# Performance work log

Measured on AMD Instinct MI355X. Metric: run time of the kernel, lower is better.

## Reference

```python
import jax, jax.numpy as jnp
import numpy as np

N, n, d = 4, 2048, 1024


def setup_inputs() -> dict:
    key = jax.random.key(0)
    k1, k2, k3, k4 = jax.random.split(key, 4)
    x = jax.random.normal(k1, (N, n, d), dtype=jnp.float32)
    mask = jax.random.randint(k2, (N, n, n), 0, 2, dtype=jnp.int32)
    Wqk = jax.random.normal(k3, (d, d), dtype=jnp.float32) * (d ** -0.5)
    Wvc = jax.random.normal(k4, (d, d), dtype=jnp.float32) * (d ** -0.5)
    return {"x": x, "mask": mask, "Wqk": Wqk, "Wvc": Wvc}


def reference(x, mask, Wqk, Wvc):
    # q = Wqk(x): torch Linear computes x @ W^T
    q = jnp.einsum('bnd,ed->bne', x, Wqk)          # [N, n, d]
    scale = jnp.asarray(x.shape[-1], x.dtype) ** 0.5
    scores = jnp.einsum('bnd,bmd->bnm', q, x) / scale  # [N, n, n]
    scores = jnp.where(mask == 0, jnp.asarray(-1e20, scores.dtype), scores)
    attention = jax.nn.softmax(scores, axis=-1)
    attended = jnp.einsum('bnm,bmd->bnd', attention, x)
    return jnp.einsum('bnd,ed->bne', attended, Wvc)
```

## Files before the change

### kernel.cpp

```cpp
#include <hip/hip_runtime.h>
#include <hip/hip_bf16.h>

typedef short bf16x8 __attribute__((ext_vector_type(8)));
typedef short s16x4  __attribute__((ext_vector_type(4)));
typedef short s16x8  __attribute__((ext_vector_type(8)));
typedef float f32x4  __attribute__((ext_vector_type(4)));

static __device__ __forceinline__ void async_cp16(const void* g, void* l) {
  __builtin_amdgcn_global_load_lds(
      (const __attribute__((address_space(1))) unsigned int*)g,
      (__attribute__((address_space(3))) unsigned int*)l, 16, 0, 0);
}

static __device__ __forceinline__ unsigned short f2bf_bits(float f) {
  union { __hip_bfloat16 b; unsigned short u; } cv;
  cv.b = __float2bfloat16(f);
  return cv.u;
}
static __device__ __forceinline__ float bf2f(short u) {
  union { float f; unsigned v; } cv;
  cv.v = ((unsigned)(unsigned short)u) << 16;
  return cv.f;
}

#define BAR() __builtin_amdgcn_s_barrier()
#define VMW(n) do { asm volatile("s_waitcnt vmcnt(" #n ")" ::: "memory"); __builtin_amdgcn_sched_barrier(0); } while (0)

__global__ __launch_bounds__(256) void cvt_f32_to_bf16(const float* __restrict__ in,
                                                       __hip_bfloat16* __restrict__ out) {
  const long i = ((long)blockIdx.x * 256 + threadIdx.x) * 4;
  const float4 v = *(const float4*)(in + i);
  s16x4 o;
  o[0] = (short)f2bf_bits(v.x);
  o[1] = (short)f2bf_bits(v.y);
  o[2] = (short)f2bf_bits(v.z);
  o[3] = (short)f2bf_bits(v.w);
  *(s16x4*)(out + i) = o;
}

struct GemmDesc {
  const __hip_bfloat16* A; const __hip_bfloat16* B; void* C;
  int lda, ldb, ldc, nT, tpb; long sA, sB, sC; float cscale;
};

template<int MODE, int BM_, int BK_>
__global__ __launch_bounds__(1024, 4) void gemm16(GemmDesc g0, GemmDesc g1, int nb0, int K) {
  constexpr int MR = BM_ / 64;
  constexpr int KR = BK_ / 32;
  constexpr int W  = BK_ * 2;
  constexpr int NB = (256 * W) / 16384;
  constexpr int BUFSZ = 16384 + NB * 16384;
  constexpr int KW = 1 + NB;
  __shared__ char lds[3 * BUFSZ];

  const int bid = blockIdx.x, nwg = gridDim.x;
  const int wg = (bid & 7) * (nwg >> 3) + (bid >> 3);
  GemmDesc g = (wg < nb0) ? g0 : g1;
  const int id = (wg < nb0) ? wg : wg - nb0;
  const int bz = id / g.tpb, tl = id - bz * g.tpb;
  const int bm = tl / g.nT, bn = tl - bm * g.nT;
  const long m0 = (long)bm * BM_, n0 = (long)bn * 256;
  const __hip_bfloat16* Ab = g.A + bz * g.sA;
  const __hip_bfloat16* Bb = g.B + bz * g.sB;

  const int t = threadIdx.x;
  const int lane = t & 63, w = t >> 6;
  const int wm = w >> 2, wn = w & 3;
  const int lr = lane & 15, cs = lane >> 4;

  const int rA  = t / (W / 16);
  const int dsl = t % (W / 16);
  const int ssl = dsl ^ ((W == 64) ? ((rA >> 1) & 3) : (rA & 7));
  const __hip_bfloat16* aSt  = Ab + (m0 + rA) * g.lda + ssl * 8;
  const __hip_bfloat16* bSt0 = Bb + (n0 + rA) * g.ldb + ssl * 8;
  const __hip_bfloat16* bSt1 = Bb + (n0 + 128 + rA) * g.ldb + ssl * 8;

  const int axor = (W == 64) ? (((lr >> 1) & 3) << 4) : ((lr & 7) << 4);
  int aRd[MR][KR], bRd[4][KR];
  #pragma unroll
  for (int mm = 0; mm < MR; ++mm)
    #pragma unroll
    for (int ks = 0; ks < KR; ++ks)
      aRd[mm][ks] = (wm * (BM_ / 4) + mm * 16 + lr) * W + ((((ks * 4 + cs) << 4) ^ axor));
  #pragma unroll
  for (int nf = 0; nf < 4; ++nf)
    #pragma unroll
    for (int ks = 0; ks < KR; ++ks)
      bRd[nf][ks] = 16384 + (wn * 64 + nf * 16 + lr) * W + ((((ks * 4 + cs) << 4) ^ axor));

  f32x4 acc[MR][4] = {};

  #define STAGE(kt, base) do { \
    async_cp16(aSt + (long)(kt) * BK_, lds + (base) + t * 16); \
    async_cp16(bSt0 + (long)(kt) * BK_, lds + (base) + 16384 + t * 16); \
    if (NB == 2) async_cp16(bSt1 + (long)(kt) * BK_, lds + (base) + 32768 + t * 16); \
  } while (0)
  #define VM_KW() do { if constexpr (KW == 2) { VMW(2); } else { VMW(3); } } while (0)

  const int nt = K / BK_;
  STAGE(0, 0);
  STAGE(1, BUFSZ);
  VM_KW();
  BAR();

  int rb = 0, sb = 2 * BUFSZ;
  for (int tt = 0; tt < nt; ++tt) {
    bf16x8 af[MR][KR], bq[4][KR];
    #pragma unroll
    for (int mm = 0; mm < MR; ++mm)
      #pragma unroll
      for (int ks = 0; ks < KR; ++ks)
        af[mm][ks] = *(const bf16x8*)(lds + rb + aRd[mm][ks]);
    #pragma unroll
    for (int nf = 0; nf < 4; ++nf)
      #pragma unroll
      for (int ks = 0; ks < KR; ++ks)
        bq[nf][ks] = *(const bf16x8*)(lds + rb + bRd[nf][ks]);
    if (tt + 2 < nt) STAGE(tt + 2, sb);
    #pragma unroll
    for (int ks = 0; ks < KR; ++ks)
      #pragma unroll
      for (int mm = 0; mm < MR; ++mm)
        #pragma unroll
        for (int nf = 0; nf < 4; ++nf)
          acc[mm][nf] = __builtin_amdgcn_mfma_f32_16x16x32_bf16(af[mm][ks], bq[nf][ks], acc[mm][nf], 0, 0, 0);
    if (tt + 2 < nt) { VM_KW(); } else { VMW(0); }
    BAR();
    rb = (rb == 2 * BUFSZ) ? 0 : rb + BUFSZ;
    sb = (sb == 2 * BUFSZ) ? 0 : sb + BUFSZ;
  }
  #undef STAGE
  #undef VM_KW

  const long crow0 = m0 + wm * (BM_ / 4) + cs * 4;
  const long ccol0 = n0 + wn * 64 + lr;
  if (MODE == 0) {
    float* C = (float*)g.C + bz * g.sC;
    #pragma unroll
    for (int mm = 0; mm < MR; ++mm)
      #pragma unroll
      for (int nf = 0; nf < 4; ++nf)
        #pragma unroll
        for (int rr = 0; rr < 4; ++rr)
          C[(crow0 + mm * 16 + rr) * g.ldc + ccol0 + nf * 16] = acc[mm][nf][rr];
  } else {
    __hip_bfloat16* C = (__hip_bfloat16*)g.C + bz * g.sC;
    #pragma unroll
    for (int mm = 0; mm < MR; ++mm)
      #pragma unroll
      for (int nf = 0; nf < 4; ++nf)
        #pragma unroll
        for (int rr = 0; rr < 4; ++rr)
          C[(crow0 + mm * 16 + rr) * g.ldc + ccol0 + nf * 16] =
              __float2bfloat16(acc[mm][nf][rr] * g.cscale);
  }
}

__global__ __launch_bounds__(256) void softmax_rows(__hip_bfloat16* __restrict__ S,
                                                    const int* __restrict__ Mask) {
  const long row = blockIdx.x;
  short* srow = (short*)(S + row * 2048);
  const int* mrow = Mask + row * 2048;
  const int t = threadIdx.x;
  const s16x8 sv = *(const s16x8*)(srow + t * 8);
  const int4 q0 = *(const int4*)(mrow + t * 8);
  const int4 q1 = *(const int4*)(mrow + t * 8 + 4);
  float f[8];
  f[0] = q0.x ? bf2f(sv[0]) : -1e20f;
  f[1] = q0.y ? bf2f(sv[1]) : -1e20f;
  f[2] = q0.z ? bf2f(sv[2]) : -1e20f;
  f[3] = q0.w ? bf2f(sv[3]) : -1e20f;
  f[4] = q1.x ? bf2f(sv[4]) : -1e20f;
  f[5] = q1.y ? bf2f(sv[5]) : -1e20f;
  f[6] = q1.z ? bf2f(sv[6]) : -1e20f;
  f[7] = q1.w ? bf2f(sv[7]) : -1e20f;

  float mx = f[0];
  #pragma unroll
  for (int i = 1; i < 8; ++i) mx = fmaxf(mx, f[i]);
  #pragma unroll
  for (int off = 32; off > 0; off >>= 1) mx = fmaxf(mx, __shfl_xor(mx, off));
  __shared__ float redm[4], reds[4];
  if ((t & 63) == 0) redm[t >> 6] = mx;
  __syncthreads();
  mx = fmaxf(fmaxf(redm[0], redm[1]), fmaxf(redm[2], redm[3]));

  float e[8];
  float s = 0.f;
  #pragma unroll
  for (int i = 0; i < 8; ++i) { e[i] = __expf(f[i] - mx); s += e[i]; }
  #pragma unroll
  for (int off = 32; off > 0; off >>= 1) s += __shfl_xor(s, off);
  if ((t & 63) == 0) reds[t >> 6] = s;
  __syncthreads();
  s = reds[0] + reds[1] + reds[2] + reds[3];
  const float inv = 1.f / s;

  s16x8 o;
  #pragma unroll
  for (int i = 0; i < 8; ++i) o[i] = (short)f2bf_bits(e[i] * inv);
  *(s16x8*)(srow + t * 8) = o;
}

extern "C" void kernel_launch(void* const* d_in, const int* in_sizes, int n_in,
                              void* d_out, int out_size, void* d_ws, size_t ws_size,
                              hipStream_t stream) {
  const float* x   = (const float*)d_in[0];
  const int*   msk = (const int*)d_in[1];
  const float* Wqk = (const float*)d_in[2];
  const float* Wvc = (const float*)d_in[3];
  float* out = (float*)d_out;
  char* ws = (char*)d_ws;

  __hip_bfloat16* xb   = (__hip_bfloat16*)(ws + 0);
  __hip_bfloat16* qb   = (__hip_bfloat16*)(ws + 16777216);
  __hip_bfloat16* vT   = (__hip_bfloat16*)(ws + 33554432);
  __hip_bfloat16* wqkb = (__hip_bfloat16*)(ws + 50331648);
  __hip_bfloat16* wvcb = (__hip_bfloat16*)(ws + 52428800);
  __hip_bfloat16* Sbf  = (__hip_bfloat16*)(ws + 54525952);

  cvt_f32_to_bf16<<<8192, 256, 0, stream>>>(x,   xb);
  cvt_f32_to_bf16<<<1024, 256, 0, stream>>>(Wqk, wqkb);
  cvt_f32_to_bf16<<<1024, 256, 0, stream>>>(Wvc, wvcb);

  GemmDesc gq{xb,   wqkb, qb, 1024, 1024, 1024, 4, 128, 0L, 0L, 0L, 0.03125f};
  GemmDesc gv{wvcb, xb,   vT, 1024, 1024, 2048, 8, 32, 0L, 2097152L, 2097152L, 1.f};
  gemm16<1, 256, 32><<<dim3(256), 1024, 0, stream>>>(gq, gv, 128, 1024);

  GemmDesc gs{qb, xb, Sbf, 1024, 1024, 2048, 8, 64, 2097152L, 2097152L, 4194304L, 1.f};
  gemm16<1, 256, 32><<<dim3(256), 1024, 0, stream>>>(gs, gs, 256, 1024);

  softmax_rows<<<dim3(8192), 256, 0, stream>>>(Sbf, msk);

  GemmDesc go{Sbf, vT, out, 2048, 2048, 1024, 4, 64, 4194304L, 2097152L, 2097152L, 1.f};
  gemm16<0, 128, 64><<<dim3(256), 1024, 0, stream>>>(go, go, 256, 2048);
}
```

Measured before the change: 144.3 us.

## Switch GEMMs to 8-wave blocks with larger per-wave tiles and fuse conversions

Replaces the 16-wave GEMM with an 8-wave kernel in which each wave computes a larger output tile (8x4 or 4x4 MFMA fragments) at BK=32. This is meant to raise MFMA work per LDS read and cut barrier cost. The output GEMM changes from a 128x256 tile at BK=64 to 256x128 at BK=32. The three f32-to-bf16 conversion launches are merged into one kernel to save launch overhead. The larger accumulator sets raise register pressure and may limit occupancy.

```diff
diff --git a/kernel.cpp b/kernel.cpp
--- a/kernel.cpp
+++ b/kernel.cpp
@@ -26,9 +26,20 @@
 #define BAR() __builtin_amdgcn_s_barrier()
 #define VMW(n) do { asm volatile("s_waitcnt vmcnt(" #n ")" ::: "memory"); __builtin_amdgcn_sched_barrier(0); } while (0)
 
-__global__ __launch_bounds__(256) void cvt_f32_to_bf16(const float* __restrict__ in,
-                                                       __hip_bfloat16* __restrict__ out) {
-  const long i = ((long)blockIdx.x * 256 + threadIdx.x) * 4;
+__global__ __launch_bounds__(256) void cvt_all(const float* __restrict__ x,
+                                               const float* __restrict__ wqk,
+                                               const float* __restrict__ wvc,
+                                               __hip_bfloat16* __restrict__ xb,
+                                               __hip_bfloat16* __restrict__ wqkb,
+                                               __hip_bfloat16* __restrict__ wvcb) {
+  const int b = blockIdx.x;
+  const float* in;
+  __hip_bfloat16* out;
+  long base;
+  if (b < 8192)       { in = x;   out = xb;   base = (long)b * 1024; }
+  else if (b < 9216)  { in = wqk; out = wqkb; base = (long)(b - 8192) * 1024; }
+  else                { in = wvc; out = wvcb; base = (long)(b - 9216) * 1024; }
+  const long i = base + threadIdx.x * 4;
   const float4 v = *(const float4*)(in + i);
   s16x4 o;
   o[0] = (short)f2bf_bits(v.x);
@@ -43,14 +54,13 @@
   int lda, ldb, ldc, nT, tpb; long sA, sB, sC; float cscale;
 };
 
-template<int MODE, int BM_, int BK_>
-__global__ __launch_bounds__(1024, 4) void gemm16(GemmDesc g0, GemmDesc g1, int nb0, int K) {
-  constexpr int MR = BM_ / 64;
-  constexpr int KR = BK_ / 32;
-  constexpr int W  = BK_ * 2;
-  constexpr int NB = (256 * W) / 16384;
-  constexpr int BUFSZ = 16384 + NB * 16384;
-  constexpr int KW = 1 + NB;
+template<int MODE, int WM, int WN, int MR_, int MINW>
+__global__ __launch_bounds__(512, MINW) void gemm8w(GemmDesc g0, GemmDesc g1, int nb0, int K) {
+  constexpr int BM    = WM * MR_ * 16;
+  constexpr int BN    = WN * 64;
+  constexpr int BOFF  = BM * 64;
+  constexpr int BUFSZ = (BM + BN) * 64;
+  constexpr int KW    = (BM + BN) / 128;
   __shared__ char lds[3 * BUFSZ];
 
   const int bid = blockIdx.x, nwg = gridDim.x;
@@ -59,45 +69,44 @@
   const int id = (wg < nb0) ? wg : wg - nb0;
   const int bz = id / g.tpb, tl = id - bz * g.tpb;
   const int bm = tl / g.nT, bn = tl - bm * g.nT;
-  const long m0 = (long)bm * BM_, n0 = (long)bn * 256;
+  const long m0 = (long)bm * BM, n0 = (long)bn * BN;
   const __hip_bfloat16* Ab = g.A + bz * g.sA;
   const __hip_bfloat16* Bb = g.B + bz * g.sB;
 
   const int t = threadIdx.x;
   const int lane = t & 63, w = t >> 6;
-  const int wm = w >> 2, wn = w & 3;
+  const int wm = w / WN, wn = w % WN;
   const int lr = lane & 15, cs = lane >> 4;
 
-  const int rA  = t / (W / 16);
-  const int dsl = t % (W / 16);
-  const int ssl = dsl ^ ((W == 64) ? ((rA >> 1) & 3) : (rA & 7));
-  const __hip_bfloat16* aSt  = Ab + (m0 + rA) * g.lda + ssl * 8;
+  const int rA  = t >> 2;
+  const int dsl = t & 3;
+  const int ssl = dsl ^ ((rA >> 1) & 3);
+  const __hip_bfloat16* aSt0 = Ab + (m0 + rA) * g.lda + ssl * 8;
+  const __hip_bfloat16* aSt1 = Ab + (m0 + 128 + rA) * g.lda + ssl * 8;
   const __hip_bfloat16* bSt0 = Bb + (n0 + rA) * g.ldb + ssl * 8;
   const __hip_bfloat16* bSt1 = Bb + (n0 + 128 + rA) * g.ldb + ssl * 8;
 
-  const int axor = (W == 64) ? (((lr >> 1) & 3) << 4) : ((lr & 7) << 4);
-  int aRd[MR][KR], bRd[4][KR];
-  #pragma unroll
-  for (int mm = 0; mm < MR; ++mm)
-    #pragma unroll
-    for (int ks = 0; ks < KR; ++ks)
-      aRd[mm][ks] = (wm * (BM_ / 4) + mm * 16 + lr) * W + ((((ks * 4 + cs) << 4) ^ axor));
+  const int axor = ((lr >> 1) & 3) << 4;
+  int aRd[MR_], bRd[4];
+  #pragma unroll
+  for (int mm = 0; mm < MR_; ++mm)
+    aRd[mm] = (wm * (MR_ * 16) + mm * 16 + lr) * 64 + ((cs << 4) ^ axor);
   #pragma unroll
   for (int nf = 0; nf < 4; ++nf)
-    #pragma unroll
-    for (int ks = 0; ks < KR; ++ks)
-      bRd[nf][ks] = 16384 + (wn * 64 + nf * 16 + lr) * W + ((((ks * 4 + cs) << 4) ^ axor));
-
-  f32x4 acc[MR][4] = {};
+    bRd[nf] = BOFF + (wn * 64 + nf * 16 + lr) * 64 + ((cs << 4) ^ axor);
+
+  f32x4 acc[MR_][4] = {};
 
   #define STAGE(kt, base) do { \
-    async_cp16(aSt + (long)(kt) * BK_, lds + (base) + t * 16); \
-    async_cp16(bSt0 + (long)(kt) * BK_, lds + (base) + 16384 + t * 16); \
-    if (NB == 2) async_cp16(bSt1 + (long)(kt) * BK_, lds + (base) + 32768 + t * 16); \
+    async_cp16(aSt0 + (long)(kt) * 32, lds + (base) + t * 16); \
+    async_cp16(aSt1 + (long)(kt) * 32, lds + (base) + 8192 + t * 16); \
+    async_cp16(bSt0 + (long)(kt) * 32, lds + (base) + BOFF + t * 16); \
+    if constexpr (BN == 256) \
+      async_cp16(bSt1 + (long)(kt) * 32, lds + (base) + BOFF + 8192 + t * 16); \
   } while (0)
-  #define VM_KW() do { if constexpr (KW == 2) { VMW(2); } else { VMW(3); } } while (0)
-
-  const int nt = K / BK_;
+  #define VM_KW() do { if constexpr (KW == 4) { VMW(4); } else { VMW(3); } } while (0)
+
+  const int nt = K >> 5;
   STAGE(0, 0);
   STAGE(1, BUFSZ);
   VM_KW();
@@ -105,25 +114,19 @@
 
   int rb = 0, sb = 2 * BUFSZ;
   for (int tt = 0; tt < nt; ++tt) {
-    bf16x8 af[MR][KR], bq[4][KR];
-    #pragma unroll
-    for (int mm = 0; mm < MR; ++mm)
+    bf16x8 af[MR_], bq[4];
+    #pragma unroll
+    for (int mm = 0; mm < MR_; ++mm)
+      af[mm] = *(const bf16x8*)(lds + rb + aRd[mm]);
+    #pragma unroll
+    for (int nf = 0; nf < 4; ++nf)
+      bq[nf] = *(const bf16x8*)(lds + rb + bRd[nf]);
+    if (tt + 2 < nt) STAGE(tt + 2, sb);
+    #pragma unroll
+    for (int mm = 0; mm < MR_; ++mm)
       #pragma unroll
-      for (int ks = 0; ks < KR; ++ks)
-        af[mm][ks] = *(const bf16x8*)(lds + rb + aRd[mm][ks]);
-    #pragma unroll
-    for (int nf = 0; nf < 4; ++nf)
-      #pragma unroll
-      for (int ks = 0; ks < KR; ++ks)
-        bq[nf][ks] = *(const bf16x8*)(lds + rb + bRd[nf][ks]);
-    if (tt + 2 < nt) STAGE(tt + 2, sb);
-    #pragma unroll
-    for (int ks = 0; ks < KR; ++ks)
-      #pragma unroll
-      for (int mm = 0; mm < MR; ++mm)
-        #pragma unroll
-        for (int nf = 0; nf < 4; ++nf)
-          acc[mm][nf] = __builtin_amdgcn_mfma_f32_16x16x32_bf16(af[mm][ks], bq[nf][ks], acc[mm][nf], 0, 0, 0);
+      for (int nf = 0; nf < 4; ++nf)
+        acc[mm][nf] = __builtin_amdgcn_mfma_f32_16x16x32_bf16(af[mm], bq[nf], acc[mm][nf], 0, 0, 0);
     if (tt + 2 < nt) { VM_KW(); } else { VMW(0); }
     BAR();
     rb = (rb == 2 * BUFSZ) ? 0 : rb + BUFSZ;
@@ -132,12 +135,12 @@
   #undef STAGE
   #undef VM_KW
 
-  const long crow0 = m0 + wm * (BM_ / 4) + cs * 4;
+  const long crow0 = m0 + wm * (MR_ * 16) + cs * 4;
   const long ccol0 = n0 + wn * 64 + lr;
   if (MODE == 0) {
     float* C = (float*)g.C + bz * g.sC;
     #pragma unroll
-    for (int mm = 0; mm < MR; ++mm)
+    for (int mm = 0; mm < MR_; ++mm)
       #pragma unroll
       for (int nf = 0; nf < 4; ++nf)
         #pragma unroll
@@ -146,7 +149,7 @@
   } else {
     __hip_bfloat16* C = (__hip_bfloat16*)g.C + bz * g.sC;
     #pragma unroll
-    for (int mm = 0; mm < MR; ++mm)
+    for (int mm = 0; mm < MR_; ++mm)
       #pragma unroll
       for (int nf = 0; nf < 4; ++nf)
         #pragma unroll
@@ -219,19 +222,17 @@
   __hip_bfloat16* wvcb = (__hip_bfloat16*)(ws + 52428800);
   __hip_bfloat16* Sbf  = (__hip_bfloat16*)(ws + 54525952);
 
-  cvt_f32_to_bf16<<<8192, 256, 0, stream>>>(x,   xb);
-  cvt_f32_to_bf16<<<1024, 256, 0, stream>>>(Wqk, wqkb);
-  cvt_f32_to_bf16<<<1024, 256, 0, stream>>>(Wvc, wvcb);
+  cvt_all<<<dim3(10240), 256, 0, stream>>>(x, Wqk, Wvc, xb, wqkb, wvcb);
 
   GemmDesc gq{xb,   wqkb, qb, 1024, 1024, 1024, 4, 128, 0L, 0L, 0L, 0.03125f};
   GemmDesc gv{wvcb, xb,   vT, 1024, 1024, 2048, 8, 32, 0L, 2097152L, 2097152L, 1.f};
-  gemm16<1, 256, 32><<<dim3(256), 1024, 0, stream>>>(gq, gv, 128, 1024);
+  gemm8w<1, 2, 4, 8, 2><<<dim3(256), 512, 0, stream>>>(gq, gv, 128, 1024);
 
   GemmDesc gs{qb, xb, Sbf, 1024, 1024, 2048, 8, 64, 2097152L, 2097152L, 4194304L, 1.f};
-  gemm16<1, 256, 32><<<dim3(256), 1024, 0, stream>>>(gs, gs, 256, 1024);
+  gemm8w<1, 2, 4, 8, 2><<<dim3(256), 512, 0, stream>>>(gs, gs, 256, 1024);
 
   softmax_rows<<<dim3(8192), 256, 0, stream>>>(Sbf, msk);
 
-  GemmDesc go{Sbf, vT, out, 2048, 2048, 1024, 4, 64, 4194304L, 2097152L, 2097152L, 1.f};
-  gemm16<0, 128, 64><<<dim3(256), 1024, 0, stream>>>(go, go, 256, 2048);
-}
+  GemmDesc go{Sbf, vT, out, 2048, 2048, 1024, 8, 64, 4194304L, 2097152L, 2097152L, 1.f};
+  gemm8w<0, 4, 2, 4, 4><<<dim3(256), 512, 0, stream>>>(go, go, 256, 2048);
+}
```

New measurement: 145.2 us. No clear change (+0.6%).
